# Kernel tuning notes

Measured on AMD Instinct MI355X. Metric: run time of the kernel, lower is better.

Reference implementation:

```python
import jax, jax.numpy as jnp
import numpy as np

E, D, H = 8, 2048, 2048  # num_experts, features, expert_dim
B, L, K = 2, 2048, 2


def setup_inputs() -> dict:
    key = jax.random.key(0)
    k1, k2, k3, k4, k5, k6 = jax.random.split(key, 6)
    x = jax.random.normal(k1, (B, L, D), dtype=jnp.float32)
    w = jax.random.uniform(k2, (B, L, K), dtype=jnp.float32)
    weights = w / jnp.sum(w, axis=-1, keepdims=True)  # normalised routing weights
    expert_indices = jax.random.randint(k3, (B, L, K), 0, E, dtype=jnp.int64)
    gate_up = jax.random.normal(k4, (E, D, 2 * H), dtype=jnp.float32) * 0.02
    down = jax.random.normal(k5, (E, H, D), dtype=jnp.float32) * 0.02
    per_expert_scale = 1.0 + 0.01 * jax.random.normal(k6, (E,), dtype=jnp.float32)
    return {"x": x, "weights": weights, "expert_indices": expert_indices,
            "gate_up": gate_up, "down": down, "per_expert_scale": per_expert_scale}


def reference(x, weights, expert_indices, gate_up, down, per_expert_scale):
    Bb, Ll, Dd = x.shape
    Ee = gate_up.shape[0]
    N = Bb * Ll
    xf = x.reshape(N, Dd)                                   # [N, D]
    idx = expert_indices.reshape(N, -1)                     # [N, K]
    wts = weights.reshape(N, -1)                            # [N, K]
    # combine[n, e] = sum_k weights[n,k] * 1[idx[n,k]==e]; scale folded in.
    onehot = jax.nn.one_hot(idx, Ee, dtype=x.dtype)         # [N, K, E]
    combine = jnp.einsum('nk,nke->ne', wts, onehot) * per_expert_scale  # [N, E]
    # Dense per-expert GatedMLP (grouped GEMM across all experts).
    h = jnp.einsum('nd,edh->enh', xf, gate_up)              # [E, N, 2H]
    gate, up = jnp.split(h, 2, axis=-1)
    act = jax.nn.gelu(gate, approximate=False) * up         # exact gelu, as torch F.gelu
    y = jnp.einsum('enh,ehd->end', act, down)               # [E, N, D]
    out = jnp.einsum('end,ne->nd', y, combine)              # weighted combine over experts
    return out.reshape(Bb, Ll, Dd)
```

## Files before the change

kernel.cpp:

```cpp
#include <hip/hip_runtime.h>
#include <math.h>

#define EXPERTS 8
#define DDIM 2048
#define HDIM 2048
#define NTOK 4096
#define NPAIR 8192
#define MAXSLOT 10240
#define MAXTILE 72

typedef _Float16 f16;
typedef __attribute__((ext_vector_type(8))) _Float16 f16x8;
typedef __attribute__((ext_vector_type(2))) _Float16 f16x2;
typedef __attribute__((ext_vector_type(4))) float f32x4;

#define GUPT_OFF 0ull
#define Y_OFF    0ull
#define DWNT_OFF 41943040ull
#define XF_OFF   134217728ull
#define ACT_OFF  150994944ull
#define CTRL_OFF 192937984ull
#define CTRL_INTS 28840

#define BARRIER() asm volatile("s_barrier" ::: "memory")
#define VMCNT4()  asm volatile("s_waitcnt vmcnt(4)" ::: "memory")
#define VMCNT0()  asm volatile("s_waitcnt vmcnt(0)" ::: "memory")

__device__ __forceinline__ void gload_lds16(const void* g, void* l) {
  __builtin_amdgcn_global_load_lds(
      (const __attribute__((address_space(1))) unsigned int*)g,
      (__attribute__((address_space(3))) unsigned int*)l,
      16, 0, 0);
}

__global__ void k_detect(const int* __restrict__ w, int* flag) {
  int i = blockIdx.x * blockDim.x + threadIdx.x;
  if (i < NPAIR / 2 && w[2 * i + 1] != 0) atomicOr(flag, 1);
}

__device__ __forceinline__ int expert_of(const int* idx, int is32, int p) {
  return is32 ? idx[p] : idx[2 * p];
}

__global__ void k_count(const int* __restrict__ idx, const int* __restrict__ flag,
                        int* cnt) {
  int p = blockIdx.x * blockDim.x + threadIdx.x;
  if (p < NPAIR) atomicAdd(&cnt[expert_of(idx, *flag, p)], 1);
}

__global__ void k_plan(const int* __restrict__ cnt, int* cursor,
                       int* tile_e, int* tile_r0, int* n_tiles) {
  if (blockIdx.x == 0 && threadIdx.x == 0) {
    int off = 0, nt = 0;
    for (int e = 0; e < EXPERTS; ++e) {
      cursor[e] = off;
      int t = (cnt[e] + 127) >> 7;
      for (int i = 0; i < t; ++i) { tile_e[nt] = e; tile_r0[nt] = off + i * 128; ++nt; }
      off += t * 128;
    }
    *n_tiles = nt;
  }
}

__global__ void k_assign(const int* __restrict__ idx, const int* __restrict__ flag,
                         const float* __restrict__ wts, const float* __restrict__ scale,
                         int* cursor, int* slot_tok, int* tok_slot, float* slot_w) {
  int p = blockIdx.x * blockDim.x + threadIdx.x;
  if (p < NPAIR) {
    int e = expert_of(idx, *flag, p);
    int pos = atomicAdd(&cursor[e], 1);
    slot_tok[pos] = p >> 1;
    tok_slot[p] = pos;
    slot_w[pos] = wts[p] * scale[e];
  }
}

__global__ void k_cvt_x(const float* __restrict__ in, f16* __restrict__ out) {
  int i = blockIdx.x * blockDim.x + threadIdx.x;
  float4 v = ((const float4*)in)[i];
  typedef __attribute__((ext_vector_type(4))) _Float16 f16x4;
  f16x4 o = {(f16)v.x, (f16)v.y, (f16)v.z, (f16)v.w};
  ((f16x4*)out)[i] = o;
}

__global__ void k_transpose(const float* __restrict__ in, f16* __restrict__ out,
                            int R, int C) {
  __shared__ float t[32][33];
  const size_t base = (size_t)blockIdx.z * R * C;
  const float* ip = in + base;
  f16* op = out + base;
  int c0 = blockIdx.x * 32, r0 = blockIdx.y * 32;
  int tx = threadIdx.x, ty = threadIdx.y;
#pragma unroll
  for (int i = 0; i < 32; i += 8)
    t[ty + i][tx] = ip[(size_t)(r0 + ty + i) * C + c0 + tx];
  __syncthreads();
  const int p = tx & 15, h = tx >> 4;
#pragma unroll
  for (int i = 0; i < 2; ++i) {
    const int j = ty + h * 8 + i * 16;
    f16x2 v = {(f16)t[2 * p][j], (f16)t[2 * p + 1][j]};
    *(f16x2*)&op[(size_t)(c0 + j) * R + r0 + 2 * p] = v;
  }
}

template <int G1>
__global__ __launch_bounds__(256, 3) void k_gemm(
    const f16* __restrict__ Asrc, const f16* __restrict__ Bsrc,
    const int* __restrict__ slot_tok,
    const int* __restrict__ tile_e, const int* __restrict__ tile_r0,
    const int* __restrict__ n_tiles, f16* __restrict__ dst) {
  __shared__ __align__(16) f16 smem[3][8192];

  const int nbx = MAXTILE, nby = G1 ? 32 : 16;
  const int nwg = nbx * nby, q = nwg / 8;
  int oid = (int)(blockIdx.y * nbx + blockIdx.x);
  int nid = (oid % 8) * q + oid / 8;
  const int bx = nid % nbx, nt = nid / nbx;
  if (bx >= *n_tiles) return;
  const int e = tile_e[bx];
  const int m0 = tile_r0[bx];

  const int tid = threadIdx.x;
  const int lane = tid & 63;
  const int wv = tid >> 6;
  const int wrM = wv >> 1;
  const int wcl = wv & 1;
  const int fr = lane & 15;
  const int fhi = lane >> 4;

  const int rlb = tid >> 2;
  const int csw = (tid & 3) ^ ((rlb >> 1) & 3);
  const f16* aS[2];
  const f16* bS[2];
#pragma unroll
  for (int i = 0; i < 2; ++i) {
    size_t arow = G1 ? (size_t)slot_tok[m0 + i * 64 + rlb] : (size_t)(m0 + i * 64 + rlb);
    aS[i] = Asrc + arow * 2048 + csw * 8;
    size_t brow;
    if (G1) brow = (size_t)e * 4096 + (i ? (size_t)2048 : 0) + (size_t)nt * 64 + rlb;
    else    brow = (size_t)e * 2048 + (size_t)nt * 128 + i * 64 + rlb;
    bS[i] = Bsrc + brow * 2048 + csw * 8;
  }

  auto stage = [&](int s, int kt) {
    const size_t ko = (size_t)kt * 32;
#pragma unroll
    for (int i = 0; i < 2; ++i)
      gload_lds16(aS[i] + ko, &smem[s][i * 2048 + tid * 8]);
#pragma unroll
    for (int i = 0; i < 2; ++i)
      gload_lds16(bS[i] + ko, &smem[s][4096 + i * 2048 + tid * 8]);
  };

  f32x4 acc[4][4];
#pragma unroll
  for (int i = 0; i < 4; ++i)
#pragma unroll
    for (int j = 0; j < 4; ++j) acc[i][j] = (f32x4){0.f, 0.f, 0.f, 0.f};

  stage(0, 0);
  stage(1, 1);
  VMCNT4();
  BARRIER();

  const int NT = DDIM / 32;
  int s = 0;
  for (int kt = 0; kt < NT; ++kt) {
    int sn = s + 2; if (sn >= 3) sn -= 3;
    if (kt + 2 < NT) stage(sn, kt + 2);

    const f16* As = &smem[s][0];
    const f16* Bs = &smem[s][4096];
    f16x8 bfr[4];
#pragma unroll
    for (int ci = 0; ci < 4; ++ci) {
      const int r = wcl * 64 + ci * 16 + fr;
      bfr[ci] = *(const f16x8*)&Bs[r * 32 + ((fhi ^ ((r >> 1) & 3)) << 3)];
    }
#pragma unroll
    for (int t = 0; t < 4; ++t) {
      const int r = wrM * 64 + t * 16 + fr;
      const f16x8 af = *(const f16x8*)&As[r * 32 + ((fhi ^ ((r >> 1) & 3)) << 3)];
#pragma unroll
      for (int ci = 0; ci < 4; ++ci)
        acc[t][ci] = __builtin_amdgcn_mfma_f32_16x16x32_f16(af, bfr[ci],
                                                            acc[t][ci], 0, 0, 0);
    }
    if (kt + 3 < NT) { VMCNT4(); } else { VMCNT0(); }
    BARRIER();
    s = (s == 2) ? 0 : s + 1;
  }

  if (G1) {
    float* xb = (float*)&smem[0][0];
    if (wcl == 1) {
#pragma unroll
      for (int t = 0; t < 4; ++t)
#pragma unroll
        for (int ci = 0; ci < 4; ++ci)
#pragma unroll
          for (int rg = 0; rg < 4; ++rg)
            xb[(wrM * 64 + t * 16 + fhi * 4 + rg) * 68 + ci * 16 + fr] =
                acc[t][ci][rg];
    }
    BARRIER();
    if (wcl == 0) {
#pragma unroll
      for (int t = 0; t < 4; ++t)
#pragma unroll
        for (int ci = 0; ci < 4; ++ci)
#pragma unroll
          for (int rg = 0; rg < 4; ++rg) {
            const int row = wrM * 64 + t * 16 + fhi * 4 + rg;
            const int gc = ci * 16 + fr;
            const float u = xb[row * 68 + gc];
            const float g = acc[t][ci][rg];
            const float a = 0.5f * g * (1.0f + erff(g * 0.70710678118654752f)) * u;
            dst[(size_t)(m0 + row) * 2048 + (size_t)nt * 64 + gc] = (f16)a;
          }
    }
  } else {
#pragma unroll
    for (int t = 0; t < 4; ++t)
#pragma unroll
      for (int ci = 0; ci < 4; ++ci)
#pragma unroll
        for (int rg = 0; rg < 4; ++rg)
          dst[(size_t)(m0 + wrM * 64 + t * 16 + fhi * 4 + rg) * 2048 +
              (size_t)nt * 128 + wcl * 64 + ci * 16 + fr] = (f16)acc[t][ci][rg];
  }
}

__global__ void k_combine(const f16* __restrict__ y, const float* __restrict__ slot_w,
                          const int* __restrict__ tok_slot, float* __restrict__ out) {
  const int gid = blockIdx.x * blockDim.x + threadIdx.x;
  const int tok = gid >> 8;
  const int c = (gid & 255) * 8;
  const int s0 = tok_slot[2 * tok], s1 = tok_slot[2 * tok + 1];
  const float w0 = slot_w[s0], w1 = slot_w[s1];
  const f16x8 v0 = *(const f16x8*)&y[(size_t)s0 * 2048 + c];
  const f16x8 v1 = *(const f16x8*)&y[(size_t)s1 * 2048 + c];
  float o[8];
#pragma unroll
  for (int j = 0; j < 8; ++j) o[j] = w0 * (float)v0[j] + w1 * (float)v1[j];
  float4* op = (float4*)&out[(size_t)tok * 2048 + c];
  op[0] = (float4){o[0], o[1], o[2], o[3]};
  op[1] = (float4){o[4], o[5], o[6], o[7]};
}

extern "C" void kernel_launch(void* const* d_in, const int* in_sizes, int n_in,
                              void* d_out, int out_size, void* d_ws, size_t ws_size,
                              hipStream_t stream) {
  const float* x = (const float*)d_in[0];
  const float* wts = (const float*)d_in[1];
  const int* idx = (const int*)d_in[2];
  const float* gup = (const float*)d_in[3];
  const float* dwn = (const float*)d_in[4];
  const float* scale = (const float*)d_in[5];
  float* out = (float*)d_out;

  char* ws = (char*)d_ws;
  f16* gup_t = (f16*)(ws + GUPT_OFF);
  f16* y = (f16*)(ws + Y_OFF);
  f16* down_t = (f16*)(ws + DWNT_OFF);
  f16* xf = (f16*)(ws + XF_OFF);
  f16* act = (f16*)(ws + ACT_OFF);
  int* ctrl = (int*)(ws + CTRL_OFF);
  int* slot_tok = ctrl;
  int* tok_slot = ctrl + 10240;
  int* cnt = ctrl + 18432;
  int* cursor = ctrl + 18440;
  int* tile_e = ctrl + 18448;
  int* tile_r0 = ctrl + 18520;
  int* n_tiles = ctrl + 18592;
  int* is32 = ctrl + 18593;
  float* slot_w = (float*)(ctrl + 18600);

  hipMemsetAsync(ctrl, 0, (size_t)CTRL_INTS * sizeof(int), stream);

  k_detect<<<NPAIR / 2 / 256, 256, 0, stream>>>(idx, is32);
  k_count<<<NPAIR / 256, 256, 0, stream>>>(idx, is32, cnt);
  k_plan<<<1, 1, 0, stream>>>(cnt, cursor, tile_e, tile_r0, n_tiles);
  k_assign<<<NPAIR / 256, 256, 0, stream>>>(idx, is32, wts, scale, cursor,
                                            slot_tok, tok_slot, slot_w);
  k_cvt_x<<<NTOK * DDIM / 4 / 256, 256, 0, stream>>>(x, xf);
  k_transpose<<<dim3(4096 / 32, 2048 / 32, EXPERTS), dim3(32, 8), 0, stream>>>(
      gup, gup_t, 2048, 4096);
  k_gemm<1><<<dim3(MAXTILE, 32), 256, 0, stream>>>(xf, gup_t, slot_tok, tile_e,
                                                   tile_r0, n_tiles, act);
  k_transpose<<<dim3(2048 / 32, 2048 / 32, EXPERTS), dim3(32, 8), 0, stream>>>(
      dwn, down_t, 2048, 2048);
  k_gemm<0><<<dim3(MAXTILE, 16), 256, 0, stream>>>(act, down_t, slot_tok, tile_e,
                                                   tile_r0, n_tiles, y);
  k_combine<<<NTOK, 256, 0, stream>>>(y, slot_w, tok_slot, out);
}
```

Baseline: 525.3 us.

## Retile grouped GEMMs to 256-row tiles with 512-thread blocks and register-fused GELU

Grouped GEMM tiles grow from 128 to 256 token rows, with 512-thread workgroups of 8 waves, and the planning kernel now pads each expert to multiples of 256. In the gate/up GEMM each wave holds both the gate and up accumulators for the same columns, so GELU*up is computed straight from registers without the LDS exchange and extra barrier. The down GEMM now uses 64-column N tiles over a 32-wide grid, and the LDS swizzle and wait counts change to match. The aim is more reuse of each B tile across rows and less epilogue overhead, at the cost of more padding waste per expert and different occupancy.

```diff
diff --git a/kernel.cpp b/kernel.cpp
--- a/kernel.cpp
+++ b/kernel.cpp
@@ -7,7 +7,7 @@
 #define NTOK 4096
 #define NPAIR 8192
 #define MAXSLOT 10240
-#define MAXTILE 72
+#define MAXTILE 40
 
 typedef _Float16 f16;
 typedef __attribute__((ext_vector_type(8))) _Float16 f16x8;
@@ -20,10 +20,11 @@
 #define XF_OFF   134217728ull
 #define ACT_OFF  150994944ull
 #define CTRL_OFF 192937984ull
-#define CTRL_INTS 28840
+#define CTRL_INTS 28776
 
 #define BARRIER() asm volatile("s_barrier" ::: "memory")
-#define VMCNT4()  asm volatile("s_waitcnt vmcnt(4)" ::: "memory")
+#define VMCNT3()  asm volatile("s_waitcnt vmcnt(3)" ::: "memory")
+#define VMCNT2()  asm volatile("s_waitcnt vmcnt(2)" ::: "memory")
 #define VMCNT0()  asm volatile("s_waitcnt vmcnt(0)" ::: "memory")
 
 __device__ __forceinline__ void gload_lds16(const void* g, void* l) {
@@ -32,6 +33,8 @@
       (__attribute__((address_space(3))) unsigned int*)l,
       16, 0, 0);
 }
+
+__device__ __forceinline__ int swz(int r) { return (r + (r >> 2)) & 3; }
 
 __global__ void k_detect(const int* __restrict__ w, int* flag) {
   int i = blockIdx.x * blockDim.x + threadIdx.x;
@@ -54,9 +57,9 @@
     int off = 0, nt = 0;
     for (int e = 0; e < EXPERTS; ++e) {
       cursor[e] = off;
-      int t = (cnt[e] + 127) >> 7;
-      for (int i = 0; i < t; ++i) { tile_e[nt] = e; tile_r0[nt] = off + i * 128; ++nt; }
-      off += t * 128;
+      int t = (cnt[e] + 255) >> 8;
+      for (int i = 0; i < t; ++i) { tile_e[nt] = e; tile_r0[nt] = off + i * 256; ++nt; }
+      off += t * 256;
     }
     *n_tiles = nt;
   }
@@ -105,18 +108,19 @@
 }
 
 template <int G1>
-__global__ __launch_bounds__(256, 3) void k_gemm(
+__global__ __launch_bounds__(512, 4) void k_gemm(
     const f16* __restrict__ Asrc, const f16* __restrict__ Bsrc,
     const int* __restrict__ slot_tok,
     const int* __restrict__ tile_e, const int* __restrict__ tile_r0,
     const int* __restrict__ n_tiles, f16* __restrict__ dst) {
-  __shared__ __align__(16) f16 smem[3][8192];
-
-  const int nbx = MAXTILE, nby = G1 ? 32 : 16;
-  const int nwg = nbx * nby, q = nwg / 8;
-  int oid = (int)(blockIdx.y * nbx + blockIdx.x);
-  int nid = (oid % 8) * q + oid / 8;
-  const int bx = nid % nbx, nt = nid / nbx;
+  constexpr int NC = G1 ? 4 : 2;
+  constexpr int BUFH = 8192 + (G1 ? 128 : 64) * 32;
+  __shared__ __align__(16) f16 smem[3][BUFH];
+
+  const int q = (MAXTILE * 32) / 8;
+  int oid = (int)(blockIdx.y * MAXTILE + blockIdx.x);
+  int nid = (oid & 7) * q + (oid >> 3);
+  const int nt = nid & 31, bx = nid >> 5;
   if (bx >= *n_tiles) return;
   const int e = tile_e[bx];
   const int m0 = tile_r0[bx];
@@ -124,111 +128,104 @@
   const int tid = threadIdx.x;
   const int lane = tid & 63;
   const int wv = tid >> 6;
-  const int wrM = wv >> 1;
-  const int wcl = wv & 1;
+  const int wm = wv >> 1;
+  const int wn = wv & 1;
   const int fr = lane & 15;
   const int fhi = lane >> 4;
 
-  const int rlb = tid >> 2;
-  const int csw = (tid & 3) ^ ((rlb >> 1) & 3);
+  const int cc = tid & 3;
+  const int ar0 = tid >> 2;
   const f16* aS[2];
-  const f16* bS[2];
 #pragma unroll
   for (int i = 0; i < 2; ++i) {
-    size_t arow = G1 ? (size_t)slot_tok[m0 + i * 64 + rlb] : (size_t)(m0 + i * 64 + rlb);
-    aS[i] = Asrc + arow * 2048 + csw * 8;
+    const int rl = i * 128 + ar0;
+    size_t arow = G1 ? (size_t)slot_tok[m0 + rl] : (size_t)(m0 + rl);
+    aS[i] = Asrc + arow * 2048 + (cc ^ swz(rl)) * 8;
+  }
+  const f16* bS = nullptr;
+  if (G1 || tid < 256) {
+    const int rb = tid >> 2;
     size_t brow;
-    if (G1) brow = (size_t)e * 4096 + (i ? (size_t)2048 : 0) + (size_t)nt * 64 + rlb;
-    else    brow = (size_t)e * 2048 + (size_t)nt * 128 + i * 64 + rlb;
-    bS[i] = Bsrc + brow * 2048 + csw * 8;
+    if (G1) brow = (size_t)e * 4096 + (rb < 64 ? (size_t)(nt * 64 + rb)
+                                               : (size_t)(2048 + nt * 64 + rb - 64));
+    else    brow = (size_t)e * 2048 + nt * 64 + rb;
+    bS = Bsrc + brow * 2048 + (cc ^ swz(rb)) * 8;
   }
 
   auto stage = [&](int s, int kt) {
     const size_t ko = (size_t)kt * 32;
-#pragma unroll
-    for (int i = 0; i < 2; ++i)
-      gload_lds16(aS[i] + ko, &smem[s][i * 2048 + tid * 8]);
-#pragma unroll
-    for (int i = 0; i < 2; ++i)
-      gload_lds16(bS[i] + ko, &smem[s][4096 + i * 2048 + tid * 8]);
+    gload_lds16(aS[0] + ko, &smem[s][tid * 8]);
+    gload_lds16(aS[1] + ko, &smem[s][4096 + tid * 8]);
+    if (G1 || tid < 256) gload_lds16(bS + ko, &smem[s][8192 + tid * 8]);
   };
 
-  f32x4 acc[4][4];
+  f32x4 acc[4][NC];
 #pragma unroll
   for (int i = 0; i < 4; ++i)
 #pragma unroll
-    for (int j = 0; j < 4; ++j) acc[i][j] = (f32x4){0.f, 0.f, 0.f, 0.f};
+    for (int j = 0; j < NC; ++j) acc[i][j] = (f32x4){0.f, 0.f, 0.f, 0.f};
 
   stage(0, 0);
   stage(1, 1);
-  VMCNT4();
+  if (G1 || wv < 4) { VMCNT3(); } else { VMCNT2(); }
   BARRIER();
 
-  const int NT = DDIM / 32;
+  const int NT = 64;
   int s = 0;
   for (int kt = 0; kt < NT; ++kt) {
-    int sn = s + 2; if (sn >= 3) sn -= 3;
-    if (kt + 2 < NT) stage(sn, kt + 2);
+    int s2 = (s == 0) ? 2 : s - 1;
+    if (kt + 2 < NT) stage(s2, kt + 2);
 
     const f16* As = &smem[s][0];
-    const f16* Bs = &smem[s][4096];
-    f16x8 bfr[4];
-#pragma unroll
-    for (int ci = 0; ci < 4; ++ci) {
-      const int r = wcl * 64 + ci * 16 + fr;
-      bfr[ci] = *(const f16x8*)&Bs[r * 32 + ((fhi ^ ((r >> 1) & 3)) << 3)];
-    }
-#pragma unroll
-    for (int t = 0; t < 4; ++t) {
-      const int r = wrM * 64 + t * 16 + fr;
-      const f16x8 af = *(const f16x8*)&As[r * 32 + ((fhi ^ ((r >> 1) & 3)) << 3)];
-#pragma unroll
-      for (int ci = 0; ci < 4; ++ci)
-        acc[t][ci] = __builtin_amdgcn_mfma_f32_16x16x32_f16(af, bfr[ci],
-                                                            acc[t][ci], 0, 0, 0);
-    }
-    if (kt + 3 < NT) { VMCNT4(); } else { VMCNT0(); }
-    BARRIER();
+    const f16* Bs = &smem[s][8192];
+    f16x8 af[4];
+#pragma unroll
+    for (int mi = 0; mi < 4; ++mi) {
+      const int r = wm * 64 + mi * 16 + fr;
+      af[mi] = *(const f16x8*)&As[r * 32 + ((fhi ^ swz(r)) << 3)];
+    }
+#pragma unroll
+    for (int ci = 0; ci < NC; ++ci) {
+      int rb;
+      if (G1) rb = (ci < 2 ? 0 : 64) + (wn * 2 + (ci & 1)) * 16 + fr;
+      else    rb = (wn * 2 + ci) * 16 + fr;
+      const f16x8 b = *(const f16x8*)&Bs[rb * 32 + ((fhi ^ swz(rb)) << 3)];
+#pragma unroll
+      for (int mi = 0; mi < 4; ++mi)
+        acc[mi][ci] = __builtin_amdgcn_mfma_f32_16x16x32_f16(af[mi], b,
+                                                             acc[mi][ci], 0, 0, 0);
+    }
+    if (kt + 1 < NT) {
+      if (kt + 2 < NT) { if (G1 || wv < 4) { VMCNT3(); } else { VMCNT2(); } }
+      else { VMCNT0(); }
+      BARRIER();
+    }
     s = (s == 2) ? 0 : s + 1;
   }
 
   if (G1) {
-    float* xb = (float*)&smem[0][0];
-    if (wcl == 1) {
-#pragma unroll
-      for (int t = 0; t < 4; ++t)
-#pragma unroll
-        for (int ci = 0; ci < 4; ++ci)
-#pragma unroll
-          for (int rg = 0; rg < 4; ++rg)
-            xb[(wrM * 64 + t * 16 + fhi * 4 + rg) * 68 + ci * 16 + fr] =
-                acc[t][ci][rg];
-    }
-    BARRIER();
-    if (wcl == 0) {
-#pragma unroll
-      for (int t = 0; t < 4; ++t)
-#pragma unroll
-        for (int ci = 0; ci < 4; ++ci)
-#pragma unroll
-          for (int rg = 0; rg < 4; ++rg) {
-            const int row = wrM * 64 + t * 16 + fhi * 4 + rg;
-            const int gc = ci * 16 + fr;
-            const float u = xb[row * 68 + gc];
-            const float g = acc[t][ci][rg];
-            const float a = 0.5f * g * (1.0f + erff(g * 0.70710678118654752f)) * u;
-            dst[(size_t)(m0 + row) * 2048 + (size_t)nt * 64 + gc] = (f16)a;
-          }
-    }
+#pragma unroll
+    for (int mi = 0; mi < 4; ++mi)
+#pragma unroll
+      for (int ci = 0; ci < 2; ++ci)
+#pragma unroll
+        for (int rg = 0; rg < 4; ++rg) {
+          const int row = m0 + wm * 64 + mi * 16 + fhi * 4 + rg;
+          const int col = nt * 64 + (wn * 2 + ci) * 16 + fr;
+          const float g = acc[mi][ci][rg];
+          const float u = acc[mi][ci + 2][rg];
+          const float a = 0.5f * g * (1.0f + erff(g * 0.70710678118654752f)) * u;
+          dst[(size_t)row * 2048 + col] = (f16)a;
+        }
   } else {
 #pragma unroll
-    for (int t = 0; t < 4; ++t)
-#pragma unroll
-      for (int ci = 0; ci < 4; ++ci)
+    for (int mi = 0; mi < 4; ++mi)
+#pragma unroll
+      for (int ci = 0; ci < 2; ++ci)
 #pragma unroll
         for (int rg = 0; rg < 4; ++rg)
-          dst[(size_t)(m0 + wrM * 64 + t * 16 + fhi * 4 + rg) * 2048 +
-              (size_t)nt * 128 + wcl * 64 + ci * 16 + fr] = (f16)acc[t][ci][rg];
+          dst[(size_t)(m0 + wm * 64 + mi * 16 + fhi * 4 + rg) * 2048 +
+              nt * 64 + (wn * 2 + ci) * 16 + fr] = (f16)acc[mi][ci][rg];
   }
 }
 
@@ -272,10 +269,10 @@
   int* cnt = ctrl + 18432;
   int* cursor = ctrl + 18440;
   int* tile_e = ctrl + 18448;
-  int* tile_r0 = ctrl + 18520;
-  int* n_tiles = ctrl + 18592;
-  int* is32 = ctrl + 18593;
-  float* slot_w = (float*)(ctrl + 18600);
+  int* tile_r0 = ctrl + 18488;
+  int* n_tiles = ctrl + 18528;
+  int* is32 = ctrl + 18529;
+  float* slot_w = (float*)(ctrl + 18536);
 
   hipMemsetAsync(ctrl, 0, (size_t)CTRL_INTS * sizeof(int), stream);
 
@@ -287,11 +284,11 @@
   k_cvt_x<<<NTOK * DDIM / 4 / 256, 256, 0, stream>>>(x, xf);
   k_transpose<<<dim3(4096 / 32, 2048 / 32, EXPERTS), dim3(32, 8), 0, stream>>>(
       gup, gup_t, 2048, 4096);
-  k_gemm<1><<<dim3(MAXTILE, 32), 256, 0, stream>>>(xf, gup_t, slot_tok, tile_e,
+  k_gemm<1><<<dim3(MAXTILE, 32), 512, 0, stream>>>(xf, gup_t, slot_tok, tile_e,
                                                    tile_r0, n_tiles, act);
   k_transpose<<<dim3(2048 / 32, 2048 / 32, EXPERTS), dim3(32, 8), 0, stream>>>(
       dwn, down_t, 2048, 2048);
-  k_gemm<0><<<dim3(MAXTILE, 16), 256, 0, stream>>>(act, down_t, slot_tok, tile_e,
+  k_gemm<0><<<dim3(MAXTILE, 32), 512, 0, stream>>>(act, down_t, slot_tok, tile_e,
                                                    tile_r0, n_tiles, y);
   k_combine<<<NTOK, 256, 0, stream>>>(y, slot_w, tok_slot, out);
 }
```

Measured after the change: 551.2 us. 4.9% more time.
